# Optimization experiments

Hardware: AMD Instinct MI355X
Metric: run time of the kernel (lower is better)

The kernel has to match this reference:

```python
import jax, jax.numpy as jnp
import numpy as np

N_NODES = 100000
N_EDGES = 1600000
IN_DIM, HID_DIM, OUT_DIM = 128, 64, 1


def setup_inputs() -> dict:
    key = jax.random.key(0)
    ks = jax.random.split(key, 8)
    x = jax.random.normal(ks[0], (N_NODES, IN_DIM), dtype=jnp.float32)
    edge_index = jax.random.randint(ks[1], (2, N_EDGES), 0, N_NODES, dtype=jnp.int64)
    # Glorot-ish scaled weights
    W1 = jax.random.normal(ks[2], (IN_DIM, HID_DIM), dtype=jnp.float32) / np.sqrt(IN_DIM)
    b1 = jnp.zeros((HID_DIM,), dtype=jnp.float32)
    W2 = jax.random.normal(ks[3], (HID_DIM, HID_DIM), dtype=jnp.float32) / np.sqrt(HID_DIM)
    b2 = jnp.zeros((HID_DIM,), dtype=jnp.float32)
    W3 = jax.random.normal(ks[4], (HID_DIM, OUT_DIM), dtype=jnp.float32) / np.sqrt(HID_DIM)
    b3 = jnp.zeros((OUT_DIM,), dtype=jnp.float32)
    return {"x": x, "edge_index": edge_index, "W1": W1, "b1": b1,
            "W2": W2, "b2": b2, "W3": W3, "b3": b3}


def _gcn_norm(edge_index, num_nodes):
    # PyG gcn_norm with add_self_loops=True, edge_weight=1:
    # deg[i] = 1 (self loop) + #incoming edges at i (dst = edge_index[1])
    dst = edge_index[1]
    deg = jnp.ones((num_nodes,), dtype=jnp.float32).at[dst].add(1.0)
    dis = jnp.where(deg > 0, 1.0 / jnp.sqrt(deg), 0.0)  # deg_inv_sqrt
    return dis


def _gcn_conv(x, W, b, src, dst, dis):
    h = x @ W                                   # [N, F_out] transform first (PyG order)
    norm = dis[src] * dis[dst]                  # [E]
    msg = h[src] * norm[:, None]                # gather + scale, [E, F_out]
    out = jnp.zeros_like(h).at[dst].add(msg)    # scatter-add aggregation
    out = out + h * (dis * dis)[:, None]        # self-loop contribution
    return out + b


def reference(x, edge_index, W1, b1, W2, b2, W3, b3):
    src, dst = edge_index[0], edge_index[1]
    dis = _gcn_norm(edge_index, x.shape[0])
    h = jax.nn.relu(_gcn_conv(x, W1, b1, src, dst, dis))   # dropout = identity (eval)
    h = jax.nn.relu(_gcn_conv(h, W2, b2, src, dst, dis))
    return _gcn_conv(h, W3, b3, src, dst, dis)
```

## Files before the change

### kernel.cpp

```cpp
#include <hip/hip_runtime.h>

#define IN_DIM 128
#define HID 64
#define MAXC 400
#define EPB 2048
#define CAP 6144
#define DPT 1024

static __device__ __forceinline__ unsigned short f2bf(float f) {
    unsigned u = __float_as_uint(f);
    u += 0x7FFF + ((u >> 16) & 1);
    return (unsigned short)(u >> 16);
}

typedef short bf16x8 __attribute__((ext_vector_type(8)));
typedef float f32x4 __attribute__((ext_vector_type(4)));

__global__ __launch_bounds__(256) void k_part1(const int* __restrict__ src,
                                               const int* __restrict__ dst,
                                               int* __restrict__ cursorC,
                                               int* __restrict__ tmp1,
                                               int E, int NC) {
    __shared__ int bcnt[MAXC];
    __shared__ int bbase[MAXC];
    int tid = threadIdx.x;
    int e0 = blockIdx.x * EPB;
    int e1 = min(e0 + EPB, E);
    for (int i = tid; i < NC; i += 256) bcnt[i] = 0;
    __syncthreads();
    for (int e = e0 + tid; e < e1; e += 256) atomicAdd(&bcnt[dst[e] >> 8], 1);
    __syncthreads();
    for (int i = tid; i < NC; i += 256) {
        int c = bcnt[i];
        bbase[i] = c ? atomicAdd(&cursorC[i], c) : 0;
    }
    __syncthreads();
    for (int i = tid; i < NC; i += 256) bcnt[i] = 0;
    __syncthreads();
    for (int e = e0 + tid; e < e1; e += 256) {
        int s = src[e], d = dst[e];
        int cb = d >> 8;
        int slot = bbase[cb] + atomicAdd(&bcnt[cb], 1);
        tmp1[(size_t)cb * CAP + slot] = s | ((d & 255) << 17);
    }
}

__global__ __launch_bounds__(512) void k_cscan(const int* __restrict__ cursorC,
                                               int* __restrict__ coarseStart,
                                               int* __restrict__ rowStart,
                                               int NC, int N, int E) {
    __shared__ int tmp[512];
    int t = threadIdx.x;
    int v = (t < NC) ? cursorC[t] : 0;
    tmp[t] = v;
    __syncthreads();
    for (int off = 1; off < 512; off <<= 1) {
        int a = (t >= off) ? tmp[t - off] : 0;
        __syncthreads();
        tmp[t] += a;
        __syncthreads();
    }
    int excl = tmp[t] - v;
    if (t < NC) coarseStart[t] = excl;
    if (t == NC - 1) coarseStart[NC] = excl + v;
    if (t == 0) rowStart[N] = E;
}

__global__ __launch_bounds__(DPT) void k_degplace(const int* __restrict__ tmp1,
                                                  const int* __restrict__ cursorC,
                                                  const int* __restrict__ coarseStart,
                                                  float* __restrict__ dis,
                                                  int* __restrict__ rowStart,
                                                  int* __restrict__ esrc, int N) {
    __shared__ int hist[256];
    __shared__ int scn[256];
    __shared__ int cur[256];
    int tid = threadIdx.x;
    int cb = blockIdx.x;
    int node0 = cb << 8;
    const int cnt = cursorC[cb];
    const size_t bp = (size_t)cb * CAP;
    const int g0 = coarseStart[cb];
    if (tid < 256) hist[tid] = 0;
    __syncthreads();
    for (int i = tid; i < cnt; i += DPT)
        atomicAdd(&hist[((unsigned)tmp1[bp + i]) >> 17], 1);
    __syncthreads();
    int v = 0;
    if (tid < 256) { v = hist[tid]; scn[tid] = v; }
    __syncthreads();
    for (int off = 1; off < 256; off <<= 1) {
        int a = 0;
        if (tid < 256 && tid >= off) a = scn[tid - off];
        __syncthreads();
        if (tid < 256) scn[tid] += a;
        __syncthreads();
    }
    if (tid < 256) {
        int myStart = g0 + scn[tid] - v;
        cur[tid] = myStart;
        int node = node0 + tid;
        if (node < N) {
            dis[node] = rsqrtf((float)v + 1.0f);
            rowStart[node] = myStart;
        }
    }
    __syncthreads();
    for (int i = tid; i < cnt; i += DPT) {
        int pk = tmp1[bp + i];
        int dl = ((unsigned)pk) >> 17;
        int pos = atomicAdd(&cur[dl], 1);
        esrc[pos] = (pk & 0x1FFFF) << 7;
    }
}

template <int K, typename T>
__global__ __launch_bounds__(256) void k_mmx(const T* __restrict__ X,
                                             const float* __restrict__ W,
                                             const float* __restrict__ dis,
                                             unsigned short* __restrict__ Hbs, int N) {
    constexpr int WP = K + 8;
    __shared__ unsigned short Wt[64 * WP];
    const int tid = threadIdx.x;
    for (int i = tid; i < K * 64; i += 256) {
        int k = i >> 6, n = i & 63;
        Wt[n * WP + k] = f2bf(W[i]);
    }
    __syncthreads();
    const int lane = tid & 63;
    const int m16 = lane & 15;
    const int quad = lane >> 4;
    const int rowBase = blockIdx.x * 64 + (tid >> 6) * 16;
    const int rowc = min(rowBase + m16, N - 1);

    f32x4 acc0 = {0.f, 0.f, 0.f, 0.f};
    f32x4 acc1 = acc0, acc2 = acc0, acc3 = acc0;
    const T* xrow = X + (size_t)rowc * K;
#pragma unroll
    for (int k0 = 0; k0 < K; k0 += 32) {
        bf16x8 af;
        if constexpr (sizeof(T) == 4) {
            const float* xp = (const float*)xrow + k0 + quad * 8;
            float4 xa = *(const float4*)xp;
            float4 xb = *(const float4*)(xp + 4);
            af[0] = (short)f2bf(xa.x); af[1] = (short)f2bf(xa.y);
            af[2] = (short)f2bf(xa.z); af[3] = (short)f2bf(xa.w);
            af[4] = (short)f2bf(xb.x); af[5] = (short)f2bf(xb.y);
            af[6] = (short)f2bf(xb.z); af[7] = (short)f2bf(xb.w);
        } else {
            af = *(const bf16x8*)((const unsigned short*)xrow + k0 + quad * 8);
        }
        const unsigned short* wp = &Wt[m16 * WP + k0 + quad * 8];
        bf16x8 b0 = *(const bf16x8*)(wp);
        bf16x8 b1 = *(const bf16x8*)(wp + 16 * WP);
        bf16x8 b2 = *(const bf16x8*)(wp + 32 * WP);
        bf16x8 b3 = *(const bf16x8*)(wp + 48 * WP);
        acc0 = __builtin_amdgcn_mfma_f32_16x16x32_bf16(af, b0, acc0, 0, 0, 0);
        acc1 = __builtin_amdgcn_mfma_f32_16x16x32_bf16(af, b1, acc1, 0, 0, 0);
        acc2 = __builtin_amdgcn_mfma_f32_16x16x32_bf16(af, b2, acc2, 0, 0, 0);
        acc3 = __builtin_amdgcn_mfma_f32_16x16x32_bf16(af, b3, acc3, 0, 0, 0);
    }
#pragma unroll
    for (int reg = 0; reg < 4; ++reg) {
        int r = rowBase + quad * 4 + reg;
        if (r < N) {
            float dsc = dis[r];
            unsigned short* hp = Hbs + (size_t)r * 64 + m16;
            hp[0]  = f2bf(acc0[reg] * dsc);
            hp[16] = f2bf(acc1[reg] * dsc);
            hp[32] = f2bf(acc2[reg] * dsc);
            hp[48] = f2bf(acc3[reg] * dsc);
        }
    }
}

#define GNODE2(ACC, RA, RB)                                                    \
    {                                                                          \
        int j0 = max(RA - base, 0);                                            \
        int j1 = min(RB - base, cnt);                                          \
        int j = j0;                                                            \
        for (; j + 4 <= j1; j += 4) {                                          \
            unsigned o1 = __shfl(eoff, j + g, 64);                             \
            unsigned o2 = __shfl(eoff, j + 2 + g, 64);                         \
            unsigned d1 = *(const unsigned*)(hbase + o1);                      \
            unsigned d2 = *(const unsigned*)(hbase + o2);                      \
            ACC.x += __uint_as_float(d1 << 16);                                \
            ACC.y += __uint_as_float(d1 & 0xFFFF0000u);                        \
            ACC.x += __uint_as_float(d2 << 16);                                \
            ACC.y += __uint_as_float(d2 & 0xFFFF0000u);                        \
        }                                                                      \
        for (; j < j1; j += 2) {                                               \
            int idx = j + g;                                                   \
            bool valid = idx < j1;                                             \
            unsigned o = __shfl(eoff, valid ? idx : j0, 64);                   \
            unsigned d = *(const unsigned*)(hbase + o);                        \
            d = valid ? d : 0u;                                                \
            ACC.x += __uint_as_float(d << 16);                                 \
            ACC.y += __uint_as_float(d & 0xFFFF0000u);                         \
        }                                                                      \
    }

template <int MODE>
__global__ __launch_bounds__(256) void k_gather64(const unsigned short* __restrict__ Hbs,
                                                  const int* __restrict__ esrc,
                                                  const int* __restrict__ rowStart,
                                                  const float* __restrict__ dis,
                                                  const float* __restrict__ b,
                                                  unsigned short* __restrict__ outB,
                                                  const float* __restrict__ W3,
                                                  const float* __restrict__ b3,
                                                  float* __restrict__ colS,
                                                  float* __restrict__ outF,
                                                  int N) {
    int lane = threadIdx.x & 63;
    int l = lane & 31;
    int g = lane >> 5;
    int wave = (blockIdx.x * 256 + threadIdx.x) >> 6;
    int g0 = wave * 4;
    if (g0 >= N) return;
    const char* hbase = (const char*)Hbs + l * 4;

    int rb = rowStart[min(g0 + lane, N)];
    int R0 = __shfl(rb, 0, 64), R1 = __shfl(rb, 1, 64);
    int R2 = __shfl(rb, 2, 64), R3 = __shfl(rb, 3, 64);
    int R4 = __shfl(rb, 4, 64);
    float dv = dis[min(g0 + lane, N - 1)];
    float d0 = __shfl(dv, 0, 64), d1 = __shfl(dv, 1, 64);
    float d2 = __shfl(dv, 2, 64), d3 = __shfl(dv, 3, 64);
    float2 bl = ((const float2*)b)[l];

    float2 a0 = {0.f, 0.f}, a1 = {0.f, 0.f}, a2 = {0.f, 0.f}, a3 = {0.f, 0.f};
    {
        int n0 = (g == 0) ? g0 : min(g0 + 2, N - 1);
        int n1 = (g == 0) ? min(g0 + 1, N - 1) : min(g0 + 3, N - 1);
        unsigned s0 = *(const unsigned*)(hbase + (size_t)n0 * 128);
        unsigned s1 = *(const unsigned*)(hbase + (size_t)n1 * 128);
        float2 f0 = {__uint_as_float(s0 << 16), __uint_as_float(s0 & 0xFFFF0000u)};
        float2 f1 = {__uint_as_float(s1 << 16), __uint_as_float(s1 & 0xFFFF0000u)};
        if (g == 0) { a0 = f0; a1 = f1; } else { a2 = f0; a3 = f1; }
    }

    for (int base = R0; base < R4; base += 64) {
        int cnt = min(64, R4 - base);
        unsigned eoff = (lane < cnt) ? (unsigned)esrc[base + lane] : 0u;
        GNODE2(a0, R0, R1)
        GNODE2(a1, R1, R2)
        GNODE2(a2, R2, R3)
        GNODE2(a3, R3, R4)
    }

    a0.x += __shfl_xor(a0.x, 32, 64); a0.y += __shfl_xor(a0.y, 32, 64);
    a1.x += __shfl_xor(a1.x, 32, 64); a1.y += __shfl_xor(a1.y, 32, 64);
    a2.x += __shfl_xor(a2.x, 32, 64); a2.y += __shfl_xor(a2.y, 32, 64);
    a3.x += __shfl_xor(a3.x, 32, 64); a3.y += __shfl_xor(a3.y, 32, 64);

    float2 v0 = {fmaxf(a0.x * d0 + bl.x, 0.f), fmaxf(a0.y * d0 + bl.y, 0.f)};
    float2 v1 = {fmaxf(a1.x * d1 + bl.x, 0.f), fmaxf(a1.y * d1 + bl.y, 0.f)};
    float2 v2 = {fmaxf(a2.x * d2 + bl.x, 0.f), fmaxf(a2.y * d2 + bl.y, 0.f)};
    float2 v3 = {fmaxf(a3.x * d3 + bl.x, 0.f), fmaxf(a3.y * d3 + bl.y, 0.f)};

    if (MODE == 1) {
        unsigned p0 = (unsigned)f2bf(v0.x) | ((unsigned)f2bf(v0.y) << 16);
        unsigned p1 = (unsigned)f2bf(v1.x) | ((unsigned)f2bf(v1.y) << 16);
        unsigned p2 = (unsigned)f2bf(v2.x) | ((unsigned)f2bf(v2.y) << 16);
        unsigned p3 = (unsigned)f2bf(v3.x) | ((unsigned)f2bf(v3.y) << 16);
        unsigned* ob = (unsigned*)outB;
        if (g == 0) {
            ob[(size_t)g0 * 32 + l] = p0;
            if (g0 + 1 < N) ob[(size_t)(g0 + 1) * 32 + l] = p1;
        } else {
            if (g0 + 2 < N) ob[(size_t)(g0 + 2) * 32 + l] = p2;
            if (g0 + 3 < N) ob[(size_t)(g0 + 3) * 32 + l] = p3;
        }
    } else {
        float2 w3 = ((const float2*)W3)[l];
        float t0 = v0.x * w3.x + v0.y * w3.y;
        float t1 = v1.x * w3.x + v1.y * w3.y;
        float t2 = v2.x * w3.x + v2.y * w3.y;
        float t3 = v3.x * w3.x + v3.y * w3.y;
#pragma unroll
        for (int off = 1; off <= 16; off <<= 1) {
            t0 += __shfl_xor(t0, off, 64);
            t1 += __shfl_xor(t1, off, 64);
            t2 += __shfl_xor(t2, off, 64);
            t3 += __shfl_xor(t3, off, 64);
        }
        if (lane == 0) {
            float bb = b3[0];
            colS[g0] = t0 * d0;
            outF[g0] = t0 * d0 * d0 + bb;
            if (g0 + 1 < N) { colS[g0 + 1] = t1 * d1; outF[g0 + 1] = t1 * d1 * d1 + bb; }
            if (g0 + 2 < N) { colS[g0 + 2] = t2 * d2; outF[g0 + 2] = t2 * d2 * d2 + bb; }
            if (g0 + 3 < N) { colS[g0 + 3] = t3 * d3; outF[g0 + 3] = t3 * d3 * d3 + bb; }
        }
    }
}

__global__ __launch_bounds__(256) void k_gather1(const float* __restrict__ colS,
                                                 const int* __restrict__ esrc,
                                                 const int* __restrict__ rowStart,
                                                 const float* __restrict__ dis,
                                                 float* __restrict__ out, int N) {
    int i = blockIdx.x * 256 + threadIdx.x;
    if (i >= N) return;
    int r0 = rowStart[i], r1 = rowStart[i + 1];
    float acc = 0.0f;
    for (int e = r0; e < r1; ++e) acc += colS[((unsigned)esrc[e]) >> 7];
    out[i] += acc * dis[i];
}

extern "C" void kernel_launch(void* const* d_in, const int* in_sizes, int n_in,
                              void* d_out, int out_size, void* d_ws, size_t ws_size,
                              hipStream_t stream) {
    const float* x  = (const float*)d_in[0];
    const int*   ei = (const int*)d_in[1];
    const float* W1 = (const float*)d_in[2];
    const float* b1 = (const float*)d_in[3];
    const float* W2 = (const float*)d_in[4];
    const float* b2 = (const float*)d_in[5];
    const float* W3 = (const float*)d_in[6];
    const float* b3 = (const float*)d_in[7];
    float* out = (float*)d_out;

    const int N = in_sizes[0] / IN_DIM;
    const int E = in_sizes[1] / 2;
    const int* src = ei;
    const int* dst = ei + E;
    const int NC = (N + 255) >> 8;

    char* w = (char*)d_ws;
    auto alloc = [&](size_t bytes) {
        char* p = w;
        w += (bytes + 1023) & ~(size_t)1023;
        return p;
    };
    float*          dis        = (float*)alloc((size_t)N * 4);
    unsigned short* Hbs        = (unsigned short*)alloc((size_t)N * 64 * 2);
    unsigned short* Hb1        = (unsigned short*)alloc((size_t)N * 64 * 2);
    float*          colS       = (float*)alloc((size_t)N * 4);
    int*            rowStart   = (int*)alloc((size_t)(N + 1) * 4);
    int*            cursorC    = (int*)alloc((size_t)MAXC * 4);
    int*            coarseStart= (int*)alloc((size_t)(MAXC + 1) * 4);
    int*            esrc       = (int*)alloc((size_t)E * 4);
    int*            tmp1       = (int*)alloc((size_t)MAXC * CAP * 4);

    const int NB_N  = (N + 255) / 256;
    const int NB_MX = (N + 63) / 64;
    const int NB_G4 = ((N + 3) / 4 * 64 + 255) / 256;
    const int NB_P  = (E + EPB - 1) / EPB;

    hipMemsetAsync(cursorC, 0, (size_t)MAXC * sizeof(int), stream);
    k_part1<<<NB_P, 256, 0, stream>>>(src, dst, cursorC, tmp1, E, NC);
    k_cscan<<<1, 512, 0, stream>>>(cursorC, coarseStart, rowStart, NC, N, E);
    k_degplace<<<NC, DPT, 0, stream>>>(tmp1, cursorC, coarseStart, dis, rowStart, esrc, N);

    k_mmx<IN_DIM, float><<<NB_MX, 256, 0, stream>>>(x, W1, dis, Hbs, N);
    k_gather64<1><<<NB_G4, 256, 0, stream>>>(Hbs, esrc, rowStart, dis, b1,
                                             Hb1, nullptr, nullptr, nullptr, nullptr, N);

    k_mmx<HID, unsigned short><<<NB_MX, 256, 0, stream>>>(Hb1, W2, dis, Hbs, N);
    k_gather64<2><<<NB_G4, 256, 0, stream>>>(Hbs, esrc, rowStart, dis, b2,
                                             nullptr, W3, b3, colS, out, N);

    k_gather1<<<NB_N, 256, 0, stream>>>(colS, esrc, rowStart, dis, out, N);
}
```

Measured before the change: 270.0 us.

## Replace global-atomic coarse bucketing with two-pass histogram and per-block prefix scan

The coarse partition of edges by destination bucket now runs a separate histogram pass per edge block, a per-bucket scan over blocks, and a global scan, then scatters edges into a compact contiguous buffer at deterministic offsets. This removes the global atomics on bucket cursors, the memset, and the padded fixed-capacity scratch layout. It also raises edges per block from 2048 to 8192. In exchange it reads dst twice and adds two small kernel launches, and it limits the edge-block count to 256.

```diff
diff --git a/kernel.cpp b/kernel.cpp
--- a/kernel.cpp
+++ b/kernel.cpp
@@ -3,8 +3,8 @@
 #define IN_DIM 128
 #define HID 64
 #define MAXC 400
-#define EPB 2048
-#define CAP 6144
+#define MAXB 256
+#define EPB 8192
 #define DPT 1024
 
 static __device__ __forceinline__ unsigned short f2bf(float f) {
@@ -16,42 +16,44 @@
 typedef short bf16x8 __attribute__((ext_vector_type(8)));
 typedef float f32x4 __attribute__((ext_vector_type(4)));
 
-__global__ __launch_bounds__(256) void k_part1(const int* __restrict__ src,
-                                               const int* __restrict__ dst,
-                                               int* __restrict__ cursorC,
-                                               int* __restrict__ tmp1,
-                                               int E, int NC) {
-    __shared__ int bcnt[MAXC];
-    __shared__ int bbase[MAXC];
-    int tid = threadIdx.x;
-    int e0 = blockIdx.x * EPB;
-    int e1 = min(e0 + EPB, E);
-    for (int i = tid; i < NC; i += 256) bcnt[i] = 0;
-    __syncthreads();
-    for (int e = e0 + tid; e < e1; e += 256) atomicAdd(&bcnt[dst[e] >> 8], 1);
-    __syncthreads();
-    for (int i = tid; i < NC; i += 256) {
-        int c = bcnt[i];
-        bbase[i] = c ? atomicAdd(&cursorC[i], c) : 0;
-    }
-    __syncthreads();
-    for (int i = tid; i < NC; i += 256) bcnt[i] = 0;
-    __syncthreads();
-    for (int e = e0 + tid; e < e1; e += 256) {
-        int s = src[e], d = dst[e];
-        int cb = d >> 8;
-        int slot = bbase[cb] + atomicAdd(&bcnt[cb], 1);
-        tmp1[(size_t)cb * CAP + slot] = s | ((d & 255) << 17);
-    }
-}
-
-__global__ __launch_bounds__(512) void k_cscan(const int* __restrict__ cursorC,
+__global__ __launch_bounds__(256) void k_hist2(const int* __restrict__ dst,
+                                               int* __restrict__ hmat, int E, int NC) {
+    __shared__ int h[MAXC];
+    int tid = threadIdx.x, blk = blockIdx.x;
+    for (int i = tid; i < NC; i += 256) h[i] = 0;
+    __syncthreads();
+    int e0 = blk * EPB, e1 = min(e0 + EPB, E);
+    for (int e = e0 + tid; e < e1; e += 256) atomicAdd(&h[dst[e] >> 8], 1);
+    __syncthreads();
+    for (int i = tid; i < NC; i += 256) hmat[blk * MAXC + i] = h[i];
+}
+
+__global__ __launch_bounds__(256) void k_bktscan(int* __restrict__ hmat,
+                                                 int* __restrict__ bktTotal,
+                                                 int NBLK, int NC) {
+    __shared__ int tmp[256];
+    int cb = blockIdx.x;
+    int t = threadIdx.x;
+    int v = (t < NBLK) ? hmat[t * MAXC + cb] : 0;
+    tmp[t] = v;
+    __syncthreads();
+    for (int off = 1; off < 256; off <<= 1) {
+        int a = (t >= off) ? tmp[t - off] : 0;
+        __syncthreads();
+        tmp[t] += a;
+        __syncthreads();
+    }
+    if (t < NBLK) hmat[t * MAXC + cb] = tmp[t] - v;
+    if (t == 255) bktTotal[cb] = tmp[255];
+}
+
+__global__ __launch_bounds__(512) void k_cscan(const int* __restrict__ bktTotal,
                                                int* __restrict__ coarseStart,
                                                int* __restrict__ rowStart,
                                                int NC, int N, int E) {
     __shared__ int tmp[512];
     int t = threadIdx.x;
-    int v = (t < NC) ? cursorC[t] : 0;
+    int v = (t < NC) ? bktTotal[t] : 0;
     tmp[t] = v;
     __syncthreads();
     for (int off = 1; off < 512; off <<= 1) {
@@ -66,8 +68,30 @@
     if (t == 0) rowStart[N] = E;
 }
 
+__global__ __launch_bounds__(256) void k_part1(const int* __restrict__ src,
+                                               const int* __restrict__ dst,
+                                               const int* __restrict__ hmat,
+                                               const int* __restrict__ coarseStart,
+                                               int* __restrict__ tmp1,
+                                               int E, int NC) {
+    __shared__ int bcnt[MAXC];
+    __shared__ int bbase[MAXC];
+    int tid = threadIdx.x, blk = blockIdx.x;
+    for (int i = tid; i < NC; i += 256) {
+        bcnt[i] = 0;
+        bbase[i] = coarseStart[i] + hmat[blk * MAXC + i];
+    }
+    __syncthreads();
+    int e0 = blk * EPB, e1 = min(e0 + EPB, E);
+    for (int e = e0 + tid; e < e1; e += 256) {
+        int s = src[e], d = dst[e];
+        int cb = d >> 8;
+        int slot = bbase[cb] + atomicAdd(&bcnt[cb], 1);
+        tmp1[slot] = s | ((d & 255) << 17);
+    }
+}
+
 __global__ __launch_bounds__(DPT) void k_degplace(const int* __restrict__ tmp1,
-                                                  const int* __restrict__ cursorC,
                                                   const int* __restrict__ coarseStart,
                                                   float* __restrict__ dis,
                                                   int* __restrict__ rowStart,
@@ -78,13 +102,11 @@
     int tid = threadIdx.x;
     int cb = blockIdx.x;
     int node0 = cb << 8;
-    const int cnt = cursorC[cb];
-    const size_t bp = (size_t)cb * CAP;
-    const int g0 = coarseStart[cb];
+    const int r0 = coarseStart[cb], r1 = coarseStart[cb + 1];
     if (tid < 256) hist[tid] = 0;
     __syncthreads();
-    for (int i = tid; i < cnt; i += DPT)
-        atomicAdd(&hist[((unsigned)tmp1[bp + i]) >> 17], 1);
+    for (int i = r0 + tid; i < r1; i += DPT)
+        atomicAdd(&hist[((unsigned)tmp1[i]) >> 17], 1);
     __syncthreads();
     int v = 0;
     if (tid < 256) { v = hist[tid]; scn[tid] = v; }
@@ -97,7 +119,7 @@
         __syncthreads();
     }
     if (tid < 256) {
-        int myStart = g0 + scn[tid] - v;
+        int myStart = r0 + scn[tid] - v;
         cur[tid] = myStart;
         int node = node0 + tid;
         if (node < N) {
@@ -106,8 +128,8 @@
         }
     }
     __syncthreads();
-    for (int i = tid; i < cnt; i += DPT) {
-        int pk = tmp1[bp + i];
+    for (int i = r0 + tid; i < r1; i += DPT) {
+        int pk = tmp1[i];
         int dl = ((unsigned)pk) >> 17;
         int pos = atomicAdd(&cur[dl], 1);
         esrc[pos] = (pk & 0x1FFFF) << 7;
@@ -327,6 +349,7 @@
     const int* src = ei;
     const int* dst = ei + E;
     const int NC = (N + 255) >> 8;
+    const int NBLK = (E + EPB - 1) / EPB;
 
     char* w = (char*)d_ws;
     auto alloc = [&](size_t bytes) {
@@ -339,20 +362,21 @@
     unsigned short* Hb1        = (unsigned short*)alloc((size_t)N * 64 * 2);
     float*          colS       = (float*)alloc((size_t)N * 4);
     int*            rowStart   = (int*)alloc((size_t)(N + 1) * 4);
-    int*            cursorC    = (int*)alloc((size_t)MAXC * 4);
+    int*            bktTotal   = (int*)alloc((size_t)MAXC * 4);
     int*            coarseStart= (int*)alloc((size_t)(MAXC + 1) * 4);
+    int*            hmat       = (int*)alloc((size_t)MAXB * MAXC * 4);
     int*            esrc       = (int*)alloc((size_t)E * 4);
-    int*            tmp1       = (int*)alloc((size_t)MAXC * CAP * 4);
+    int*            tmp1       = (int*)alloc((size_t)E * 4);
 
     const int NB_N  = (N + 255) / 256;
     const int NB_MX = (N + 63) / 64;
     const int NB_G4 = ((N + 3) / 4 * 64 + 255) / 256;
-    const int NB_P  = (E + EPB - 1) / EPB;
-
-    hipMemsetAsync(cursorC, 0, (size_t)MAXC * sizeof(int), stream);
-    k_part1<<<NB_P, 256, 0, stream>>>(src, dst, cursorC, tmp1, E, NC);
-    k_cscan<<<1, 512, 0, stream>>>(cursorC, coarseStart, rowStart, NC, N, E);
-    k_degplace<<<NC, DPT, 0, stream>>>(tmp1, cursorC, coarseStart, dis, rowStart, esrc, N);
+
+    k_hist2<<<NBLK, 256, 0, stream>>>(dst, hmat, E, NC);
+    k_bktscan<<<NC, 256, 0, stream>>>(hmat, bktTotal, NBLK, NC);
+    k_cscan<<<1, 512, 0, stream>>>(bktTotal, coarseStart, rowStart, NC, N, E);
+    k_part1<<<NBLK, 256, 0, stream>>>(src, dst, hmat, coarseStart, tmp1, E, NC);
+    k_degplace<<<NC, DPT, 0, stream>>>(tmp1, coarseStart, dis, rowStart, esrc, N);
 
     k_mmx<IN_DIM, float><<<NB_MX, 256, 0, stream>>>(x, W1, dis, Hbs, N);
     k_gather64<1><<<NB_G4, 256, 0, stream>>>(Hbs, esrc, rowStart, dis, b1,
```

Result: faster. 262.7 us (-2.7%).
